# Optimization experiments

Measured on AMD Instinct MI355X. Metric: run time of the kernel, lower is better.

Reference implementation:

```python
import jax, jax.numpy as jnp
import numpy as np

N, E, DIN, HID, DOUT = 50000, 800000, 128, 128, 64
NEG_SLOPE = 0.2


def setup_inputs() -> dict:
    key = jax.random.key(0)
    ks = jax.random.split(key, 16)
    x = jax.random.normal(ks[0], (N, DIN), dtype=jnp.float32)
    edge_index = jax.random.randint(ks[1], (2, E), 0, N, dtype=jnp.int64)

    def lin(k, fan_in, fan_out):
        kw, kb = jax.random.split(k)
        s = 1.0 / np.sqrt(fan_in)
        W = jax.random.uniform(kw, (fan_in, fan_out), jnp.float32, -s, s)
        b = jax.random.uniform(kb, (fan_out,), jnp.float32, -s, s)
        return W, b

    Wl, bl = lin(ks[2], DIN, DIN)   # GATv2 lin_l
    Wr, br = lin(ks[3], DIN, DIN)   # GATv2 lin_r
    att = jax.random.uniform(ks[4], (DIN,), jnp.float32, -1.0 / np.sqrt(DIN), 1.0 / np.sqrt(DIN))
    bg = jnp.zeros((DIN,), jnp.float32)  # GAT output bias
    W1, b1 = lin(ks[5], DIN, HID)   # ChebConv K=1 -> plain linear
    W2, b2 = lin(ks[6], HID, HID)
    W3, b3 = lin(ks[7], HID, DOUT)
    return {"x": x, "edge_index": edge_index, "Wl": Wl, "bl": bl, "Wr": Wr,
            "br": br, "att": att, "bg": bg, "W1": W1, "b1": b1,
            "W2": W2, "b2": b2, "W3": W3, "b3": b3}


def reference(x, edge_index, Wl, bl, Wr, br, att, bg, W1, b1, W2, b2, W3, b3):
    n = x.shape[0]
    # GATv2Conv adds self loops by default
    loop = jnp.arange(n, dtype=edge_index.dtype)
    src = jnp.concatenate([edge_index[0], loop])  # source j
    dst = jnp.concatenate([edge_index[1], loop])  # target i

    xl = x @ Wl + bl  # [N, DIN]
    xr = x @ Wr + br  # [N, DIN]

    # GATv2 edge scores: leaky_relu(x_l[j] + x_r[i]) . att
    e = jax.nn.leaky_relu(xl[src] + xr[dst], NEG_SLOPE)  # [E+N, DIN]
    a = e @ att                                          # [E+N]

    # softmax over incoming edges of each destination node
    amax = jax.ops.segment_max(a, dst, num_segments=n)
    ea = jnp.exp(a - amax[dst])
    denom = jax.ops.segment_sum(ea, dst, num_segments=n)
    alpha = ea / denom[dst]                              # [E+N]

    # aggregate messages alpha * x_l[j] at destinations
    h = jax.ops.segment_sum(alpha[:, None] * xl[src], dst, num_segments=n) + bg

    # ChebConv with K=1 reduces to a linear layer (T_0(L) = I)
    h = jax.nn.relu(h @ W1 + b1)
    h = jax.nn.relu(h @ W2 + b2)
    # dropout_rate = 0.0 -> identity
    return h @ W3 + b3
```

## Files before the change

kernel.cpp:

```cpp
#include <hip/hip_runtime.h>
#include <hip/hip_bf16.h>

#define DIN 128
#define NEG_SLOPE 0.2f
#define PTILE 2048
#define CVT_BLKS 289

typedef __attribute__((ext_vector_type(8))) short bf16x8;
typedef __attribute__((ext_vector_type(8))) unsigned short u16x8;
typedef __attribute__((ext_vector_type(4))) float f32x4;
typedef __attribute__((ext_vector_type(2))) float f32x2;
typedef __attribute__((ext_vector_type(4))) unsigned int u32x4;

__device__ __forceinline__ ushort f2bf(float f) {
  unsigned u = __float_as_uint(f);
  u += 0x7FFFu + ((u >> 16) & 1u);
  return (ushort)(u >> 16);
}
__device__ __forceinline__ f32x2 bfpair(unsigned u) {
  f32x2 r;
  r.x = __uint_as_float(u << 16);
  r.y = __uint_as_float(u & 0xFFFF0000u);
  return r;
}

template <int CTRL>
__device__ __forceinline__ float dppadd(float x) {
  int v = __builtin_amdgcn_update_dpp(0, __float_as_int(x), CTRL, 0xf, 0xf, true);
  return x + __int_as_float(v);
}
__device__ __forceinline__ float red16(float t) {
  t = dppadd<0xB1>(t);
  t = dppadd<0x4E>(t);
  t = dppadd<0x141>(t);
  t = dppadd<0x140>(t);
  return t;
}

__global__ __launch_bounds__(256) void cvt_hist_kernel(
    const float* __restrict__ Wl, const float* __restrict__ Wr,
    const float* __restrict__ W1, const float* __restrict__ W2,
    const float* __restrict__ W3,
    ushort* __restrict__ WlT, ushort* __restrict__ WrT,
    ushort* __restrict__ W1T, ushort* __restrict__ W2T,
    ushort* __restrict__ W3T,
    const int* __restrict__ ei, int* __restrict__ nhist, int E) {
  if (blockIdx.x < CVT_BLKS) {
    int i = blockIdx.x * 256 + threadIdx.x;
    if (i < 16384) {
      int k = i >> 7, c = i & 127; WlT[c * 128 + k] = f2bf(Wl[i]);
    } else if (i < 32768) {
      int j = i - 16384; int k = j >> 7, c = j & 127; WrT[c * 128 + k] = f2bf(Wr[j]);
    } else if (i < 49152) {
      int j = i - 32768; int k = j >> 7, c = j & 127; W1T[c * 128 + k] = f2bf(W1[j]);
    } else if (i < 65536) {
      int j = i - 49152; int k = j >> 7, c = j & 127; W2T[c * 128 + k] = f2bf(W2[j]);
    } else if (i < 73728) {
      int j = i - 65536; int k = j >> 6, c = j & 63; W3T[c * 128 + k] = f2bf(W3[j]);
    }
  } else {
    int tile = (int)blockIdx.x - CVT_BLKS;
    int base = tile * PTILE;
    int lim = min(E, base + PTILE);
    for (int e = base + threadIdx.x; e < lim; e += 256)
      atomicAdd(&nhist[ei[E + e]], 1);
  }
}

__global__ __launch_bounds__(256) void scanA_kernel(
    const int* __restrict__ nhist, int* __restrict__ offsets,
    int* __restrict__ bsum, int N) {
  __shared__ int sh[256];
  int tid = threadIdx.x;
  int node = blockIdx.x * 256 + tid;
  int v = (node < N) ? nhist[node] : 0;
  sh[tid] = v;
  __syncthreads();
  for (int d = 1; d < 256; d <<= 1) {
    int t = (tid >= d) ? sh[tid - d] : 0;
    __syncthreads();
    sh[tid] += t;
    __syncthreads();
  }
  if (node < N) offsets[node] = sh[tid] - v;
  if (tid == 255) bsum[blockIdx.x] = sh[255];
}

__global__ __launch_bounds__(256) void scanB_kernel(
    const int* __restrict__ bsum, int* __restrict__ gbase,
    int* __restrict__ offsets, int N, int nbuck, int E) {
  __shared__ int sh[256];
  int tid = threadIdx.x;
  int v = (tid < nbuck) ? bsum[tid] : 0;
  sh[tid] = v;
  __syncthreads();
  for (int d = 1; d < 256; d <<= 1) {
    int t = (tid >= d) ? sh[tid - d] : 0;
    __syncthreads();
    sh[tid] += t;
    __syncthreads();
  }
  if (tid < nbuck) gbase[tid] = sh[tid] - v;
  if (tid == 0) offsets[N] = E;
}

__global__ __launch_bounds__(256) void scanC_kernel(
    int* __restrict__ offsets, const int* __restrict__ gbase,
    int* __restrict__ cursor, int N) {
  int node = blockIdx.x * 256 + threadIdx.x;
  if (node < N) {
    int o = offsets[node] + gbase[blockIdx.x];
    offsets[node] = o;
    cursor[node] = o;
  }
}

__global__ __launch_bounds__(256) void lin_scatter_kernel(
    const float* __restrict__ x,
    const ushort* __restrict__ WlT, const float* __restrict__ bl,
    const ushort* __restrict__ WrT, const float* __restrict__ br,
    ushort* __restrict__ xl, ushort* __restrict__ xr, int n, int nblk_lin,
    const int* __restrict__ ei, int* __restrict__ cursor,
    ushort* __restrict__ ssrc, int E) {
  if ((int)blockIdx.x < nblk_lin) {
    const int tid = threadIdx.x;
    const int wv = tid >> 6, lane = tid & 63;
    const int m = lane & 15, quad = lane >> 4;
    const int colbase = (wv & 1) * 64;
    const int nodew = blockIdx.x * 32 + (wv >> 1) * 16;
    int arow = nodew + m; if (arow >= n) arow = n - 1;
    f32x4 accl[4], accr[4];
#pragma unroll
    for (int nt = 0; nt < 4; nt++) { accl[nt] = (f32x4){0,0,0,0}; accr[nt] = (f32x4){0,0,0,0}; }
#pragma unroll
    for (int kk = 0; kk < 4; kk++) {
      int k0 = kk * 32 + quad * 8;
      const float4* xp = (const float4*)(x + (long)arow * 128 + k0);
      float4 x0 = xp[0], x1 = xp[1];
      bf16x8 af;
      af[0] = (short)f2bf(x0.x); af[1] = (short)f2bf(x0.y);
      af[2] = (short)f2bf(x0.z); af[3] = (short)f2bf(x0.w);
      af[4] = (short)f2bf(x1.x); af[5] = (short)f2bf(x1.y);
      af[6] = (short)f2bf(x1.z); af[7] = (short)f2bf(x1.w);
#pragma unroll
      for (int nt = 0; nt < 4; nt++) {
        int brow = colbase + nt * 16 + m;
        bf16x8 bl8 = *(const bf16x8*)(WlT + brow * 128 + k0);
        bf16x8 br8 = *(const bf16x8*)(WrT + brow * 128 + k0);
        accl[nt] = __builtin_amdgcn_mfma_f32_16x16x32_bf16(af, bl8, accl[nt], 0, 0, 0);
        accr[nt] = __builtin_amdgcn_mfma_f32_16x16x32_bf16(af, br8, accr[nt], 0, 0, 0);
      }
    }
#pragma unroll
    for (int nt = 0; nt < 4; nt++) {
      int col = colbase + nt * 16 + m;
      float vbl = bl[col], vbr = br[col];
#pragma unroll
      for (int r = 0; r < 4; r++) {
        int node = nodew + quad * 4 + r;
        if (node < n) {
          xl[(long)node * 128 + col] = f2bf(accl[nt][r] + vbl);
          xr[(long)node * 128 + col] = f2bf(accr[nt][r] + vbr);
        }
      }
    }
  } else {
    int tile = (int)blockIdx.x - nblk_lin;
    int base = tile * PTILE;
    int lim = min(E, base + PTILE);
    for (int e = base + threadIdx.x; e < lim; e += 256) {
      int s = ei[e], d = ei[E + e];
      int pos = atomicAdd(&cursor[d], 1);
      ssrc[pos] = (ushort)s;
    }
  }
}

__global__ __launch_bounds__(256) void node_aggr_kernel(
    const ushort* __restrict__ xl, const ushort* __restrict__ xr,
    const float* __restrict__ att, const float* __restrict__ bg,
    const int* __restrict__ offsets, const ushort* __restrict__ ssrc,
    ushort* __restrict__ h, int n) {
  int wave = (int)((blockIdx.x * (long)blockDim.x + threadIdx.x) >> 6);
  int lane = threadIdx.x & 63;
  if (wave >= n) return;
  const int node = wave;
  const int eg = lane >> 4, sl = lane & 15;
  const int beg = offsets[node];
  const int end = offsets[node + 1];
  const int last = end - 1;
  const ushort* __restrict__ xls = xl + sl * 8;
  int ia = beg + 2 * eg;
  bool va = ia < end, vb = ia + 1 < end;
  int sa = (int)ssrc[min(ia, last)];
  int sb = (int)ssrc[min(ia + 1, last)];
  u32x4 uva = *(const u32x4*)(xls + (long)sa * 128);
  u32x4 uvb = *(const u32x4*)(xls + (long)sb * 128);

  f32x2 a06[4], a04[4], r2[4], acc2[4];
  {
    const float4* ap = (const float4*)(att + sl * 8);
    float4 a0 = ap[0], a1 = ap[1];
    f32x2 av[4] = {{a0.x, a0.y}, {a0.z, a0.w}, {a1.x, a1.y}, {a1.z, a1.w}};
#pragma unroll
    for (int jp = 0; jp < 4; jp++) {
      a06[jp] = 0.6f * av[jp];
      a04[jp] = 0.4f * av[jp];
    }
  }
  u32x4 rv = *(const u32x4*)(xr + (long)node * 128 + sl * 8);
  u32x4 lv = *(const u32x4*)(xls + (long)node * 128);
  float denom;
  {
    f32x2 t1 = {0.f, 0.f}, t2 = {0.f, 0.f};
    f32x2 l2[4];
#pragma unroll
    for (int jp = 0; jp < 4; jp++) {
      r2[jp] = bfpair(rv[jp]);
      l2[jp] = bfpair(lv[jp]);
      f32x2 v = l2[jp] + r2[jp];
      t1 += a06[jp] * v;
      t2 += a04[jp] * __builtin_elementwise_abs(v);
    }
    float t = red16(t1.x + t1.y + t2.x + t2.y);
    float es = __expf(t);
    denom = (eg == 0) ? es : 0.f;
#pragma unroll
    for (int jp = 0; jp < 4; jp++)
      acc2[jp] = (eg == 0) ? es * l2[jp] : (f32x2){0.f, 0.f};
  }
  for (int p = beg; p < end; p += 8) {
    u32x4 ca = uva, cb = uvb;
    bool cva = va, cvb = vb;
    int ian = p + 8 + 2 * eg;
    va = ian < end; vb = ian + 1 < end;
    sa = (int)ssrc[min(ian, last)];
    sb = (int)ssrc[min(ian + 1, last)];
    uva = *(const u32x4*)(xls + (long)sa * 128);
    uvb = *(const u32x4*)(xls + (long)sb * 128);
    f32x2 ua2[4], ub2[4];
    f32x2 ta1 = {0.f, 0.f}, ta2 = {0.f, 0.f};
    f32x2 tb1 = {0.f, 0.f}, tb2 = {0.f, 0.f};
#pragma unroll
    for (int jp = 0; jp < 4; jp++) {
      ua2[jp] = bfpair(ca[jp]);
      ub2[jp] = bfpair(cb[jp]);
      f32x2 va2 = ua2[jp] + r2[jp];
      f32x2 vb2 = ub2[jp] + r2[jp];
      ta1 += a06[jp] * va2;
      ta2 += a04[jp] * __builtin_elementwise_abs(va2);
      tb1 += a06[jp] * vb2;
      tb2 += a04[jp] * __builtin_elementwise_abs(vb2);
    }
    float ta = red16(ta1.x + ta1.y + ta2.x + ta2.y);
    float tb = red16(tb1.x + tb1.y + tb2.x + tb2.y);
    float ea = cva ? __expf(ta) : 0.f;
    float eb = cvb ? __expf(tb) : 0.f;
    denom += ea + eb;
#pragma unroll
    for (int jp = 0; jp < 4; jp++)
      acc2[jp] += ea * ua2[jp] + eb * ub2[jp];
  }
#pragma unroll
  for (int jp = 0; jp < 4; jp++) {
    acc2[jp].x += __shfl_xor(acc2[jp].x, 16);
    acc2[jp].y += __shfl_xor(acc2[jp].y, 16);
    acc2[jp].x += __shfl_xor(acc2[jp].x, 32);
    acc2[jp].y += __shfl_xor(acc2[jp].y, 32);
  }
  denom += __shfl_xor(denom, 16);
  denom += __shfl_xor(denom, 32);
  if (eg == 0) {
    float inv = 1.0f / denom;
    const float4* bp = (const float4*)(bg + sl * 8);
    float4 g0 = bp[0], g1 = bp[1];
    f32x2 gv[4] = {{g0.x, g0.y}, {g0.z, g0.w}, {g1.x, g1.y}, {g1.z, g1.w}};
    u16x8 o;
#pragma unroll
    for (int jp = 0; jp < 4; jp++) {
      f32x2 hv = acc2[jp] * inv + gv[jp];
      o[2 * jp]     = f2bf(hv.x);
      o[2 * jp + 1] = f2bf(hv.y);
    }
    *(u16x8*)(h + (long)node * 128 + sl * 8) = o;
  }
}

#define LDSP 136
__global__ __launch_bounds__(256) void mlp_mfma_kernel(
    const ushort* __restrict__ hb,
    const ushort* __restrict__ W1T, const float* __restrict__ b1,
    const ushort* __restrict__ W2T, const float* __restrict__ b2,
    const ushort* __restrict__ W3T, const float* __restrict__ b3,
    float* __restrict__ out, int n) {
  __shared__ ushort act[32][LDSP];
  const int tid = threadIdx.x;
  const int wv = tid >> 6, lane = tid & 63;
  const int m = lane & 15, quad = lane >> 4;
  const int half = wv & 1, ng = wv >> 1;
  const int colbase = half * 64;
  const int nodew = blockIdx.x * 32 + ng * 16;
  int arow = nodew + m; if (arow >= n) arow = n - 1;
  f32x4 acc[4];
#pragma unroll
  for (int nt = 0; nt < 4; nt++) acc[nt] = (f32x4){0,0,0,0};
#pragma unroll
  for (int kk = 0; kk < 4; kk++) {
    int k0 = kk * 32 + quad * 8;
    bf16x8 af = *(const bf16x8*)(hb + (long)arow * 128 + k0);
#pragma unroll
    for (int nt = 0; nt < 4; nt++) {
      bf16x8 b8 = *(const bf16x8*)(W1T + (colbase + nt * 16 + m) * 128 + k0);
      acc[nt] = __builtin_amdgcn_mfma_f32_16x16x32_bf16(af, b8, acc[nt], 0, 0, 0);
    }
  }
#pragma unroll
  for (int nt = 0; nt < 4; nt++) {
    int col = colbase + nt * 16 + m;
    float b = b1[col];
#pragma unroll
    for (int r = 0; r < 4; r++)
      act[ng * 16 + quad * 4 + r][col] = f2bf(fmaxf(acc[nt][r] + b, 0.f));
  }
  __syncthreads();
#pragma unroll
  for (int nt = 0; nt < 4; nt++) acc[nt] = (f32x4){0,0,0,0};
#pragma unroll
  for (int kk = 0; kk < 4; kk++) {
    int k0 = kk * 32 + quad * 8;
    bf16x8 af = *(const bf16x8*)(&act[ng * 16 + m][k0]);
#pragma unroll
    for (int nt = 0; nt < 4; nt++) {
      bf16x8 b8 = *(const bf16x8*)(W2T + (colbase + nt * 16 + m) * 128 + k0);
      acc[nt] = __builtin_amdgcn_mfma_f32_16x16x32_bf16(af, b8, acc[nt], 0, 0, 0);
    }
  }
  __syncthreads();
#pragma unroll
  for (int nt = 0; nt < 4; nt++) {
    int col = colbase + nt * 16 + m;
    float b = b2[col];
#pragma unroll
    for (int r = 0; r < 4; r++)
      act[ng * 16 + quad * 4 + r][col] = f2bf(fmaxf(acc[nt][r] + b, 0.f));
  }
  __syncthreads();
  f32x4 acc3[2];
#pragma unroll
  for (int nt = 0; nt < 2; nt++) acc3[nt] = (f32x4){0,0,0,0};
#pragma unroll
  for (int kk = 0; kk < 4; kk++) {
    int k0 = kk * 32 + quad * 8;
    bf16x8 af = *(const bf16x8*)(&act[ng * 16 + m][k0]);
#pragma unroll
    for (int nt = 0; nt < 2; nt++) {
      bf16x8 b8 = *(const bf16x8*)(W3T + (half * 32 + nt * 16 + m) * 128 + k0);
      acc3[nt] = __builtin_amdgcn_mfma_f32_16x16x32_bf16(af, b8, acc3[nt], 0, 0, 0);
    }
  }
#pragma unroll
  for (int nt = 0; nt < 2; nt++) {
    int col = half * 32 + nt * 16 + m;
    float b = b3[col];
#pragma unroll
    for (int r = 0; r < 4; r++) {
      int node = nodew + quad * 4 + r;
      if (node < n) out[(long)node * 64 + col] = acc3[nt][r] + b;
    }
  }
}

extern "C" void kernel_launch(void* const* d_in, const int* in_sizes, int n_in,
                              void* d_out, int out_size, void* d_ws, size_t ws_size,
                              hipStream_t stream) {
  const float* x   = (const float*)d_in[0];
  const int*   ei  = (const int*)d_in[1];
  const float* Wl  = (const float*)d_in[2];
  const float* bl  = (const float*)d_in[3];
  const float* Wr  = (const float*)d_in[4];
  const float* br  = (const float*)d_in[5];
  const float* att = (const float*)d_in[6];
  const float* bg  = (const float*)d_in[7];
  const float* W1  = (const float*)d_in[8];
  const float* b1  = (const float*)d_in[9];
  const float* W2  = (const float*)d_in[10];
  const float* b2  = (const float*)d_in[11];
  const float* W3  = (const float*)d_in[12];
  const float* b3  = (const float*)d_in[13];
  float* out = (float*)d_out;

  const int N = in_sizes[0] / DIN;
  const int E = in_sizes[1] / 2;
  const int nbuck = (N + 255) >> 8;

  char* ws = (char*)d_ws;
  size_t off = 0;
  auto alloc = [&](size_t bytes) {
    void* p = ws + off;
    off += (bytes + 255) & ~(size_t)255;
    return p;
  };
  int* bsum      = (int*)alloc(256 * 4);
  int* gbase     = (int*)alloc(256 * 4);
  int* nhist     = (int*)alloc((size_t)N * 4);
  int* cursor    = (int*)alloc((size_t)N * 4);
  int* offsets   = (int*)alloc(((size_t)N + 4) * 4);
  ushort* ssrc   = (ushort*)alloc(((size_t)E + 16) * 2);
  ushort* xlb    = (ushort*)alloc((size_t)N * DIN * 2);
  ushort* xrb    = (ushort*)alloc((size_t)N * DIN * 2);
  ushort* hbf    = (ushort*)alloc((size_t)N * DIN * 2);
  ushort* WlT    = (ushort*)alloc(16384 * 2);
  ushort* WrT    = (ushort*)alloc(16384 * 2);
  ushort* W1T    = (ushort*)alloc(16384 * 2);
  ushort* W2T    = (ushort*)alloc(16384 * 2);
  ushort* W3T    = (ushort*)alloc(8192 * 2);
  (void)ws_size;

  hipMemsetAsync(nhist, 0, (size_t)N * 4, stream);

  int ntile = (E + PTILE - 1) / PTILE;
  cvt_hist_kernel<<<CVT_BLKS + ntile, 256, 0, stream>>>(
      Wl, Wr, W1, W2, W3, WlT, WrT, W1T, W2T, W3T, ei, nhist, E);

  scanA_kernel<<<nbuck, 256, 0, stream>>>(nhist, offsets, bsum, N);
  scanB_kernel<<<1, 256, 0, stream>>>(bsum, gbase, offsets, N, nbuck, E);
  scanC_kernel<<<nbuck, 256, 0, stream>>>(offsets, gbase, cursor, N);

  int nblk32 = (N + 31) / 32;
  lin_scatter_kernel<<<nblk32 + ntile, 256, 0, stream>>>(
      x, WlT, bl, WrT, br, xlb, xrb, N, nblk32, ei, cursor, ssrc, E);

  int nwblk = (N + 3) / 4;
  node_aggr_kernel<<<nwblk, 256, 0, stream>>>(xlb, xrb, att, bg,
                                              offsets, ssrc, hbf, N);

  mlp_mfma_kernel<<<nblk32, 256, 0, stream>>>(hbf, W1T, b1, W2T, b2,
                                              W3T, b3, out, N);
}
```

Before: 283.6 us.

## Bucket-partition edges by destination before CSR scatter and merge scan kernels

Edges are no longer scattered into CSR order with global atomics on per-node cursors directly. Each tile now groups its edges by destination bucket (256 nodes per bucket) in shared memory and writes them to a bucket-contiguous staging buffer. A new per-bucket scatter kernel then places them, so cursor atomics and ssrc writes stay in a small address window. The scanB and scanC kernels are also merged into one launch. The cost is an extra pass over a 4-byte-per-edge buffer and another launch. The scatter also runs on only one block per bucket, and the larger shared-memory footprint is reserved for the MFMA blocks of the same kernel.

```diff
diff --git a/kernel.cpp b/kernel.cpp
--- a/kernel.cpp
+++ b/kernel.cpp
@@ -86,10 +86,11 @@
   if (tid == 255) bsum[blockIdx.x] = sh[255];
 }
 
-__global__ __launch_bounds__(256) void scanB_kernel(
-    const int* __restrict__ bsum, int* __restrict__ gbase,
-    int* __restrict__ offsets, int N, int nbuck, int E) {
-  __shared__ int sh[256];
+__global__ __launch_bounds__(256) void scanBC_kernel(
+    const int* __restrict__ bsum, int* __restrict__ offsets,
+    int* __restrict__ cursor, int* __restrict__ cum,
+    int* __restrict__ cursorB, int N, int nbuck, int E) {
+  __shared__ int sh[256], ex[256];
   int tid = threadIdx.x;
   int v = (tid < nbuck) ? bsum[tid] : 0;
   sh[tid] = v;
@@ -100,28 +101,28 @@
     sh[tid] += t;
     __syncthreads();
   }
-  if (tid < nbuck) gbase[tid] = sh[tid] - v;
-  if (tid == 0) offsets[N] = E;
-}
-
-__global__ __launch_bounds__(256) void scanC_kernel(
-    int* __restrict__ offsets, const int* __restrict__ gbase,
-    int* __restrict__ cursor, int N) {
-  int node = blockIdx.x * 256 + threadIdx.x;
+  ex[tid] = sh[tid] - v;
+  __syncthreads();
+  int node = (int)blockIdx.x * 256 + tid;
   if (node < N) {
-    int o = offsets[node] + gbase[blockIdx.x];
+    int o = offsets[node] + ex[blockIdx.x];
     offsets[node] = o;
     cursor[node] = o;
   }
-}
-
-__global__ __launch_bounds__(256) void lin_scatter_kernel(
+  if (blockIdx.x == 0) {
+    cum[tid] = ex[tid];
+    cursorB[tid] = ex[tid];
+    if (tid == 0) offsets[N] = E;
+  }
+}
+
+__global__ __launch_bounds__(256) void lin_partition_kernel(
     const float* __restrict__ x,
     const ushort* __restrict__ WlT, const float* __restrict__ bl,
     const ushort* __restrict__ WrT, const float* __restrict__ br,
     ushort* __restrict__ xl, ushort* __restrict__ xr, int n, int nblk_lin,
-    const int* __restrict__ ei, int* __restrict__ cursor,
-    ushort* __restrict__ ssrc, int E) {
+    const int* __restrict__ ei, unsigned* __restrict__ part,
+    int* __restrict__ cursorB, int E) {
   if ((int)blockIdx.x < nblk_lin) {
     const int tid = threadIdx.x;
     const int wv = tid >> 6, lane = tid & 63;
@@ -165,14 +166,61 @@
       }
     }
   } else {
-    int tile = (int)blockIdx.x - nblk_lin;
-    int base = tile * PTILE;
-    int lim = min(E, base + PTILE);
-    for (int e = base + threadIdx.x; e < lim; e += 256) {
+    __shared__ int hist[256], pref[256], sexcl[256], curs[256], gbase[256];
+    __shared__ unsigned buf[PTILE];
+    const int tid = threadIdx.x;
+    const int tile0 = ((int)blockIdx.x - nblk_lin) * PTILE;
+    const int tcount = min(PTILE, E - tile0);
+    hist[tid] = 0;
+    __syncthreads();
+    unsigned pk[PTILE / 256];
+    int cnt = 0;
+    for (int i = tid; i < tcount; i += 256) {
+      int e = tile0 + i;
       int s = ei[e], d = ei[E + e];
-      int pos = atomicAdd(&cursor[d], 1);
-      ssrc[pos] = (ushort)s;
-    }
+      unsigned p = ((unsigned)d << 16) | (unsigned)s;
+      pk[cnt++] = p;
+      atomicAdd(&hist[d >> 8], 1);
+    }
+    __syncthreads();
+    int v = hist[tid];
+    pref[tid] = v;
+    __syncthreads();
+    for (int d = 1; d < 256; d <<= 1) {
+      int t = (tid >= d) ? pref[tid - d] : 0;
+      __syncthreads();
+      pref[tid] += t;
+      __syncthreads();
+    }
+    int exc = pref[tid] - v;
+    sexcl[tid] = exc;
+    curs[tid] = exc;
+    gbase[tid] = (v > 0) ? atomicAdd(&cursorB[tid], v) : 0;
+    __syncthreads();
+    for (int j = 0; j < cnt; j++) {
+      int b = pk[j] >> 24;
+      int pos = atomicAdd(&curs[b], 1);
+      buf[pos] = pk[j];
+    }
+    __syncthreads();
+    for (int i = tid; i < tcount; i += 256) {
+      unsigned p = buf[i];
+      int b = p >> 24;
+      part[gbase[b] + (i - sexcl[b])] = p;
+    }
+  }
+}
+
+__global__ __launch_bounds__(256) void scatter_kernel(
+    const unsigned* __restrict__ part, const int* __restrict__ cum,
+    int* __restrict__ cursor, ushort* __restrict__ ssrc) {
+  const int b = blockIdx.x;
+  const int beg = cum[b], end = cum[b + 1];
+  for (int i = beg + threadIdx.x; i < end; i += 256) {
+    unsigned p = part[i];
+    int d = p >> 16;
+    int pos = atomicAdd(&cursor[d], 1);
+    ssrc[pos] = (ushort)(p & 0xFFFFu);
   }
 }
 
@@ -401,10 +449,12 @@
     return p;
   };
   int* bsum      = (int*)alloc(256 * 4);
-  int* gbase     = (int*)alloc(256 * 4);
+  int* cum       = (int*)alloc(260 * 4);
+  int* cursorB   = (int*)alloc(256 * 4);
   int* nhist     = (int*)alloc((size_t)N * 4);
   int* cursor    = (int*)alloc((size_t)N * 4);
   int* offsets   = (int*)alloc(((size_t)N + 4) * 4);
+  unsigned* part = (unsigned*)alloc((size_t)E * 4);
   ushort* ssrc   = (ushort*)alloc(((size_t)E + 16) * 2);
   ushort* xlb    = (ushort*)alloc((size_t)N * DIN * 2);
   ushort* xrb    = (ushort*)alloc((size_t)N * DIN * 2);
@@ -423,12 +473,14 @@
       Wl, Wr, W1, W2, W3, WlT, WrT, W1T, W2T, W3T, ei, nhist, E);
 
   scanA_kernel<<<nbuck, 256, 0, stream>>>(nhist, offsets, bsum, N);
-  scanB_kernel<<<1, 256, 0, stream>>>(bsum, gbase, offsets, N, nbuck, E);
-  scanC_kernel<<<nbuck, 256, 0, stream>>>(offsets, gbase, cursor, N);
+  scanBC_kernel<<<nbuck, 256, 0, stream>>>(bsum, offsets, cursor, cum,
+                                           cursorB, N, nbuck, E);
 
   int nblk32 = (N + 31) / 32;
-  lin_scatter_kernel<<<nblk32 + ntile, 256, 0, stream>>>(
-      x, WlT, bl, WrT, br, xlb, xrb, N, nblk32, ei, cursor, ssrc, E);
+  lin_partition_kernel<<<nblk32 + ntile, 256, 0, stream>>>(
+      x, WlT, bl, WrT, br, xlb, xrb, N, nblk32, ei, part, cursorB, E);
+
+  scatter_kernel<<<nbuck, 256, 0, stream>>>(part, cum, cursor, ssrc);
 
   int nwblk = (N + 3) / 4;
   node_aggr_kernel<<<nwblk, 256, 0, stream>>>(xlb, xrb, att, bg,
```

Result: faster. 274.1 us (-3.3%).
